# Optimization experiments

Measured on AMD Instinct MI355X. Metric: run time of the kernel, lower is better.

## Reference

```python
import jax, jax.numpy as jnp
import numpy as np

TOP_K = 2


def setup_inputs() -> dict:
    key = jax.random.key(0)
    k1, k2, k3 = jax.random.split(key, 3)
    inp = jax.random.normal(k1, (16384, 2048), dtype=jnp.float32)
    W = jax.random.normal(k2, (64, 2048), dtype=jnp.float32) * 0.02
    b = jax.random.normal(k3, (64,), dtype=jnp.float32) * 0.02
    return {"inp": inp, "W": W, "b": b}


def reference(inp, W, b):
    # gate logits: [tokens, num_expert]
    gate = jnp.einsum("td,ed->te", inp, W) + b
    # top-k over experts (lax.top_k returns sorted; torch used sorted=False,
    # so results match up to a per-token permutation of the k slots)
    top_val, top_idx = jax.lax.top_k(gate, TOP_K)  # [tokens, k]
    gate_score = jax.nn.softmax(top_val, axis=-1)[:, None, :]  # [tokens, 1, k]
    gate_top_k_idx = top_idx.reshape(-1)  # [tokens * k]
    return (gate_top_k_idx, gate_score)
```

## Files before the change

kernel.cpp:

```cpp
#include <hip/hip_runtime.h>
#include <math.h>


#define KDIM 2048
#define NEXP 64
#define TM 64
#define BK 32
#define LDSS 68

__global__ __launch_bounds__(256) void gate_partial_kernel(
    const float* __restrict__ inp,
    const float* __restrict__ W,
    float* __restrict__ partial,
    int tokens, int kPerSplit)
{
    __shared__ float As[BK][LDSS];
    __shared__ float Ws[BK][LDSS];

    const int tid = threadIdx.x;
    const int tx  = tid & 15;
    const int ty  = tid >> 4;
    const int tokBase = blockIdx.x * TM;
    const int split   = blockIdx.y;
    const int k0      = split * kPerSplit;

    const int lrow = tid >> 3;
    const int lcol = (tid & 7) << 2;

    const float* aPtr0 = inp + (size_t)(tokBase + lrow)      * KDIM + k0 + lcol;
    const float* aPtr1 = inp + (size_t)(tokBase + lrow + 32) * KDIM + k0 + lcol;
    const float* wPtr0 = W   + (size_t)lrow        * KDIM + k0 + lcol;
    const float* wPtr1 = W   + (size_t)(lrow + 32) * KDIM + k0 + lcol;

    float4 aReg0 = *(const float4*)(aPtr0);
    float4 aReg1 = *(const float4*)(aPtr1);
    float4 wReg0 = *(const float4*)(wPtr0);
    float4 wReg1 = *(const float4*)(wPtr1);

    float acc[4][4];
    #pragma unroll
    for (int r = 0; r < 4; ++r)
        #pragma unroll
        for (int c = 0; c < 4; ++c) acc[r][c] = 0.0f;

    const int NT = kPerSplit / BK;
    for (int kt = 0; kt < NT; ++kt) {
        __syncthreads();
        #pragma unroll
        for (int c = 0; c < 4; ++c) {
            As[lcol + c][lrow]      = ((const float*)&aReg0)[c];
            As[lcol + c][lrow + 32] = ((const float*)&aReg1)[c];
            Ws[lcol + c][lrow]      = ((const float*)&wReg0)[c];
            Ws[lcol + c][lrow + 32] = ((const float*)&wReg1)[c];
        }
        __syncthreads();
        if (kt + 1 < NT) {
            const int off = (kt + 1) * BK;
            aReg0 = *(const float4*)(aPtr0 + off);
            aReg1 = *(const float4*)(aPtr1 + off);
            wReg0 = *(const float4*)(wPtr0 + off);
            wReg1 = *(const float4*)(wPtr1 + off);
        }
        #pragma unroll 8
        for (int kk = 0; kk < BK; ++kk) {
            const float4 av = *(const float4*)&As[kk][ty << 2];
            const float4 wv = *(const float4*)&Ws[kk][tx << 2];
            const float a[4] = {av.x, av.y, av.z, av.w};
            const float w[4] = {wv.x, wv.y, wv.z, wv.w};
            #pragma unroll
            for (int r = 0; r < 4; ++r)
                #pragma unroll
                for (int c = 0; c < 4; ++c)
                    acc[r][c] = fmaf(a[r], w[c], acc[r][c]);
        }
    }

    const int eBase = tx << 2;
    #pragma unroll
    for (int r = 0; r < 4; ++r) {
        const int token = tokBase + (ty << 2) + r;
        float4 v = make_float4(acc[r][0], acc[r][1], acc[r][2], acc[r][3]);
        *(float4*)&partial[((size_t)split * tokens + token) * NEXP + eBase] = v;
    }
}

__global__ __launch_bounds__(256) void reduce_topk_kernel(
    const float* __restrict__ partial,
    const float* __restrict__ bias,
    float* __restrict__ out,
    int tokens, int S)
{
    const int tid = threadIdx.x;
    const int tx  = tid & 15;
    const int ty  = tid >> 4;
    const int token = blockIdx.x * 16 + ty;
    const int eBase = tx << 2;

    float4 v = make_float4(0.f, 0.f, 0.f, 0.f);
    for (int s = 0; s < S; ++s) {
        const float4 p = *(const float4*)&partial[((size_t)s * tokens + token) * NEXP + eBase];
        v.x += p.x; v.y += p.y; v.z += p.z; v.w += p.w;
    }
    const float4 bv = *(const float4*)&bias[eBase];
    float g[4] = { v.x + bv.x, v.y + bv.y, v.z + bv.z, v.w + bv.w };

    float v1 = g[0]; int i1 = eBase;
    float v2 = -INFINITY; int i2 = -1;
    #pragma unroll
    for (int c = 1; c < 4; ++c) {
        const float vv = g[c];
        const int   ii = eBase + c;
        if (vv > v1)      { v2 = v1; i2 = i1; v1 = vv; i1 = ii; }
        else if (vv > v2) { v2 = vv; i2 = ii; }
    }
    #pragma unroll
    for (int m = 1; m <= 8; m <<= 1) {
        const float ov1 = __shfl_xor(v1, m);
        const int   oi1 = __shfl_xor(i1, m);
        const float ov2 = __shfl_xor(v2, m);
        const int   oi2 = __shfl_xor(i2, m);
        const bool aw = (v1 > ov1) || (v1 == ov1 && i1 < oi1);
        const float nv1 = aw ? v1  : ov1;  const int ni1 = aw ? i1  : oi1;
        const float lv  = aw ? ov1 : v1;   const int li  = aw ? oi1 : i1;
        const float sv  = aw ? v2  : ov2;  const int si  = aw ? i2  : oi2;
        const bool sw = (sv > lv) || (sv == lv && si < li);
        v1 = nv1; i1 = ni1;
        v2 = sw ? sv : lv; i2 = sw ? si : li;
    }
    if (tx == 0) {
        const float e2 = expf(v2 - v1);
        const float denom = 1.0f + e2;
        out[2 * token]     = (float)i1;
        out[2 * token + 1] = (float)i2;
        out[tokens * 2 + 2 * token]     = 1.0f / denom;
        out[tokens * 2 + 2 * token + 1] = e2 / denom;
    }
}

extern "C" void kernel_launch(void* const* d_in, const int* in_sizes, int n_in,
                              void* d_out, int out_size, void* d_ws, size_t ws_size,
                              hipStream_t stream) {
    const float* inp  = (const float*)d_in[0];
    const float* W    = (const float*)d_in[1];
    const float* bias = (const float*)d_in[2];
    float* out = (float*)d_out;
    float* partial = (float*)d_ws;

    const int tokens = in_sizes[0] / KDIM;

    int S = 4;
    while (S > 1 && (size_t)S * tokens * NEXP * sizeof(float) > ws_size) S >>= 1;
    const int kPerSplit = KDIM / S;

    dim3 grid(tokens / TM, S);
    gate_partial_kernel<<<grid, 256, 0, stream>>>(inp, W, partial, tokens, kPerSplit);
    reduce_topk_kernel<<<tokens / 16, 256, 0, stream>>>(partial, bias, out, tokens, S);
}
```

Measured before the change: 218.2 us.

## Compute all experts per thread with pre-transposed broadcast W

Each thread now owns one token and accumulates all 64 expert logits in registers. W is pre-transposed into a k-major layout so every lane reads the same W elements, which allows scalar or broadcast loads, and only the input tile is staged through LDS. The split-K factor rises to 8, and a small transpose kernel is added. This trades heavy register use and lower occupancy for far fewer LDS reads per FMA.

```diff
diff --git a/kernel.cpp b/kernel.cpp
--- a/kernel.cpp
+++ b/kernel.cpp
@@ -1,87 +1,81 @@
 #include <hip/hip_runtime.h>
 #include <math.h>
+#include <stdint.h>
 
 
 #define KDIM 2048
 #define NEXP 64
-#define TM 64
-#define BK 32
-#define LDSS 68
+#define TPB  256
+#define BK   32
+#define LDST (BK + 4)
+
+__global__ __launch_bounds__(256) void transpose_w_kernel(
+    const float* __restrict__ W, float* __restrict__ Wt)
+{
+    const int idx = blockIdx.x * 256 + threadIdx.x;
+    const int e = idx >> 11;
+    const int k = idx & 2047;
+    Wt[k * NEXP + e] = W[idx];
+}
 
 __global__ __launch_bounds__(256) void gate_partial_kernel(
     const float* __restrict__ inp,
-    const float* __restrict__ W,
+    const float* __restrict__ Wt,
     float* __restrict__ partial,
     int tokens, int kPerSplit)
 {
-    __shared__ float As[BK][LDSS];
-    __shared__ float Ws[BK][LDSS];
+    __shared__ float As[TPB * LDST];
 
-    const int tid = threadIdx.x;
-    const int tx  = tid & 15;
-    const int ty  = tid >> 4;
-    const int tokBase = blockIdx.x * TM;
+    const int tid     = threadIdx.x;
+    const int tokBase = blockIdx.x * TPB;
     const int split   = blockIdx.y;
     const int k0      = split * kPerSplit;
 
-    const int lrow = tid >> 3;
-    const int lcol = (tid & 7) << 2;
+    const int srow = tid >> 3;
+    const int scol = (tid & 7) << 2;
+    const float* aBase = inp + (size_t)tokBase * KDIM + k0;
 
-    const float* aPtr0 = inp + (size_t)(tokBase + lrow)      * KDIM + k0 + lcol;
-    const float* aPtr1 = inp + (size_t)(tokBase + lrow + 32) * KDIM + k0 + lcol;
-    const float* wPtr0 = W   + (size_t)lrow        * KDIM + k0 + lcol;
-    const float* wPtr1 = W   + (size_t)(lrow + 32) * KDIM + k0 + lcol;
+    float4 stage[8];
+    #pragma unroll
+    for (int p = 0; p < 8; ++p)
+        stage[p] = *(const float4*)(aBase + (size_t)(srow + 32 * p) * KDIM + scol);
 
-    float4 aReg0 = *(const float4*)(aPtr0);
-    float4 aReg1 = *(const float4*)(aPtr1);
-    float4 wReg0 = *(const float4*)(wPtr0);
-    float4 wReg1 = *(const float4*)(wPtr1);
-
-    float acc[4][4];
+    float acc[NEXP];
     #pragma unroll
-    for (int r = 0; r < 4; ++r)
-        #pragma unroll
-        for (int c = 0; c < 4; ++c) acc[r][c] = 0.0f;
+    for (int e = 0; e < NEXP; ++e) acc[e] = 0.0f;
 
     const int NT = kPerSplit / BK;
     for (int kt = 0; kt < NT; ++kt) {
         __syncthreads();
         #pragma unroll
-        for (int c = 0; c < 4; ++c) {
-            As[lcol + c][lrow]      = ((const float*)&aReg0)[c];
-            As[lcol + c][lrow + 32] = ((const float*)&aReg1)[c];
-            Ws[lcol + c][lrow]      = ((const float*)&wReg0)[c];
-            Ws[lcol + c][lrow + 32] = ((const float*)&wReg1)[c];
-        }
+        for (int p = 0; p < 8; ++p)
+            *(float4*)&As[(srow + 32 * p) * LDST + scol] = stage[p];
         __syncthreads();
         if (kt + 1 < NT) {
-            const int off = (kt + 1) * BK;
-            aReg0 = *(const float4*)(aPtr0 + off);
-            aReg1 = *(const float4*)(aPtr1 + off);
-            wReg0 = *(const float4*)(wPtr0 + off);
-            wReg1 = *(const float4*)(wPtr1 + off);
+            const int koff = (kt + 1) * BK;
+            #pragma unroll
+            for (int p = 0; p < 8; ++p)
+                stage[p] = *(const float4*)(aBase + (size_t)(srow + 32 * p) * KDIM + koff + scol);
         }
-        #pragma unroll 8
-        for (int kk = 0; kk < BK; ++kk) {
-            const float4 av = *(const float4*)&As[kk][ty << 2];
-            const float4 wv = *(const float4*)&Ws[kk][tx << 2];
-            const float a[4] = {av.x, av.y, av.z, av.w};
-            const float w[4] = {wv.x, wv.y, wv.z, wv.w};
+        const float* __restrict__ wTile = Wt + (size_t)(k0 + kt * BK) * NEXP;
+        #pragma unroll
+        for (int kq = 0; kq < BK / 4; ++kq) {
+            const float4 a4 = *(const float4*)&As[tid * LDST + (kq << 2)];
             #pragma unroll
-            for (int r = 0; r < 4; ++r)
+            for (int j = 0; j < 4; ++j) {
+                const float a = (j == 0) ? a4.x : (j == 1) ? a4.y : (j == 2) ? a4.z : a4.w;
+                const float* __restrict__ wr = wTile + ((kq << 2) + j) * NEXP;
                 #pragma unroll
-                for (int c = 0; c < 4; ++c)
-                    acc[r][c] = fmaf(a[r], w[c], acc[r][c]);
+                for (int e = 0; e < NEXP; ++e)
+                    acc[e] = fmaf(a, wr[e], acc[e]);
+            }
         }
     }
 
-    const int eBase = tx << 2;
+    float* p = partial + ((size_t)split * tokens + tokBase + tid) * NEXP;
     #pragma unroll
-    for (int r = 0; r < 4; ++r) {
-        const int token = tokBase + (ty << 2) + r;
-        float4 v = make_float4(acc[r][0], acc[r][1], acc[r][2], acc[r][3]);
-        *(float4*)&partial[((size_t)split * tokens + token) * NEXP + eBase] = v;
-    }
+    for (int e = 0; e < NEXP; e += 4)
+        *(float4*)&p[e] = make_float4(acc[e], acc[e + 1], acc[e + 2], acc[e + 3]);
 }
 
 __global__ __launch_bounds__(256) void reduce_topk_kernel(
@@ -144,15 +138,22 @@
     const float* W    = (const float*)d_in[1];
     const float* bias = (const float*)d_in[2];
     float* out = (float*)d_out;
-    float* partial = (float*)d_ws;
 
     const int tokens = in_sizes[0] / KDIM;
 
-    int S = 4;
-    while (S > 1 && (size_t)S * tokens * NEXP * sizeof(float) > ws_size) S >>= 1;
+    int S = 8;
+    while (S > 1 &&
+           (size_t)S * tokens * NEXP * sizeof(float) + (size_t)KDIM * NEXP * sizeof(float) > ws_size)
+        S >>= 1;
     const int kPerSplit = KDIM / S;
 
-    dim3 grid(tokens / TM, S);
-    gate_partial_kernel<<<grid, 256, 0, stream>>>(inp, W, partial, tokens, kPerSplit);
+    float* partial = (float*)d_ws;
+    float* Wt = partial + (size_t)S * tokens * NEXP;
+
+    transpose_w_kernel<<<(NEXP * KDIM) / 256, 256, 0, stream>>>(W, Wt);
+
+    dim3 grid(tokens / TPB, S);
+    gate_partial_kernel<<<grid, 256, 0, stream>>>(inp, Wt, partial, tokens, kPerSplit);
+
     reduce_topk_kernel<<<tokens / 16, 256, 0, stream>>>(partial, bias, out, tokens, S);
 }
```

Result: slower. 323.1 us (+48.1%).
